# Performance work log

Hardware: AMD Instinct MI355X
Metric: run time of the kernel (lower is better)

The kernel has to match this reference:

```python
import jax, jax.numpy as jnp
import numpy as np

DIM = 1024
N_HEADS = 16


def setup_inputs() -> dict:
    key = jax.random.key(0)
    ks = jax.random.split(key, 7)
    x = jax.random.normal(ks[0], (2, 2048, DIM), dtype=jnp.float32)
    wq = jax.random.normal(ks[1], (DIM, DIM), dtype=jnp.float32) * 0.01
    wk = jax.random.normal(ks[2], (DIM, DIM), dtype=jnp.float32) * 0.01
    wv = jax.random.normal(ks[3], (DIM, DIM), dtype=jnp.float32) * 0.01
    wo = jax.random.normal(ks[4], (DIM, DIM), dtype=jnp.float32) * 0.01
    w1 = jax.random.normal(ks[5], (DIM, 4 * DIM), dtype=jnp.float32) * 0.01
    w2 = jax.random.normal(ks[6], (4 * DIM, DIM), dtype=jnp.float32) * 0.01
    return {"x": x, "wq": wq, "wk": wk, "wv": wv, "wo": wo, "w1": w1, "w2": w2}


def reference(x, wq, wk, wv, wo, w1, w2):
    bsz, seqlen, dim = x.shape
    head_dim = dim // N_HEADS
    # project and split heads: [b, h, s, d]
    q = (x @ wq).reshape(bsz, seqlen, N_HEADS, head_dim).transpose(0, 2, 1, 3)
    k = (x @ wk).reshape(bsz, seqlen, N_HEADS, head_dim).transpose(0, 2, 1, 3)
    v = (x @ wv).reshape(bsz, seqlen, N_HEADS, head_dim).transpose(0, 2, 1, 3)
    scale = head_dim ** (-0.5)
    # full [b, h, s, s] score matrix, as in the original module
    attn = jnp.einsum('bhqd,bhkd->bhqk', q, k) * scale
    attn = jax.nn.softmax(attn, axis=-1)
    out = jnp.einsum('bhqk,bhkd->bhqd', attn, v)
    out = out.transpose(0, 2, 1, 3).reshape(bsz, seqlen, dim)
    x = x + out @ wo
    h = jax.nn.relu(x @ w1)
    x = x + h @ w2
    return x
```

## Files before the change

### kernel.cpp

```cpp
#include <hip/hip_runtime.h>
#include <hip/hip_bf16.h>
#include <stdint.h>

typedef __attribute__((ext_vector_type(8))) short short8_t;
typedef __attribute__((ext_vector_type(4))) short short4_t;
typedef __attribute__((ext_vector_type(4))) float floatx4;

#define MTOT 4096
#define DIMV 1024
#define SEQ  2048
#define NH   16
#define HD   64
#define QKV_LD 3072
#define KVB 64
#define NKT (SEQ / KVB)

__device__ __forceinline__ floatx4 mfma16(short8_t a, short8_t b, floatx4 c) {
    return __builtin_amdgcn_mfma_f32_16x16x32_bf16(a, b, c, 0, 0, 0);
}

__device__ __forceinline__ void gload_lds16(const void* g, void* l) {
    __builtin_amdgcn_global_load_lds(
        (const __attribute__((address_space(1))) void*)g,
        (__attribute__((address_space(3))) void*)l,
        16, 0, 0);
}

__device__ __forceinline__ short bf16bits(float f) {
    return __builtin_bit_cast(short, __float2bfloat16(f));
}

__device__ __forceinline__ short8_t frag64(const __hip_bfloat16* base, int row, int col0) {
    int off = row * 64 + (((col0 >> 3) ^ (row & 7)) << 3);
    return *(const short8_t*)(base + off);
}


struct bf4 { __hip_bfloat16 a, b, c, d; };

__global__ void castbf(const float* __restrict__ x, __hip_bfloat16* __restrict__ o, int n4) {
    int i = blockIdx.x * 256 + threadIdx.x;
    if (i < n4) {
        const float4* xv = reinterpret_cast<const float4*>(x) + i;
        float4 v = *xv;
        bf4 r;
        r.a = __float2bfloat16(v.x); r.b = __float2bfloat16(v.y);
        r.c = __float2bfloat16(v.z); r.d = __float2bfloat16(v.w);
        *reinterpret_cast<bf4*>(o + (size_t)i * 4) = r;
    }
}

__global__ void wtrans(const float* __restrict__ w, __hip_bfloat16* __restrict__ wt,
                       int K, int N, float scale) {
    __shared__ float tile[32][33];
    int k0 = blockIdx.x * 32, n0 = blockIdx.y * 32;
    int tx = threadIdx.x & 31, ty = threadIdx.x >> 5;
    #pragma unroll
    for (int r = 0; r < 32; r += 8)
        tile[ty + r][tx] = w[(size_t)(k0 + ty + r) * N + n0 + tx];
    __syncthreads();
    #pragma unroll
    for (int r = 0; r < 32; r += 8)
        wt[(size_t)(n0 + ty + r) * K + k0 + tx] = __float2bfloat16(tile[tx][ty + r] * scale);
}

__global__ void vtrans(const __hip_bfloat16* __restrict__ v, int ld,
                       __hip_bfloat16* __restrict__ vt) {
    __shared__ __hip_bfloat16 tile[32][33];
    int s0 = blockIdx.x * 32;
    int c0 = blockIdx.y * 32;
    int tx = threadIdx.x & 31, ty = threadIdx.x >> 5;
    #pragma unroll
    for (int r = 0; r < 32; r += 8)
        tile[ty + r][tx] = v[(size_t)(s0 + ty + r) * ld + c0 + tx];
    __syncthreads();
    int b = s0 >> 11;
    int h = c0 >> 6;
    int d0 = c0 & 63;
    #pragma unroll
    for (int r = 0; r < 32; r += 8)
        vt[(size_t)((b * NH + h) * HD + d0 + ty + r) * SEQ + (s0 & 2047) + tx] = tile[tx][ty + r];
}

__global__ void combine2(const float* __restrict__ p0, const float* __restrict__ p1,
                         const float* __restrict__ resid, float* __restrict__ out, int n4) {
    int i = blockIdx.x * 256 + threadIdx.x;
    if (i < n4) {
        float4 a = reinterpret_cast<const float4*>(p0)[i];
        float4 b = reinterpret_cast<const float4*>(p1)[i];
        float4 c = reinterpret_cast<const float4*>(resid)[i];
        float4 r;
        r.x = a.x + b.x + c.x; r.y = a.y + b.y + c.y;
        r.z = a.z + b.z + c.z; r.w = a.w + b.w + c.w;
        reinterpret_cast<float4*>(out)[i] = r;
    }
}

template <int EPI>
__launch_bounds__(256)
__global__ void gemm_bt(const __hip_bfloat16* __restrict__ A,
                        const __hip_bfloat16* __restrict__ Bt,
                        int M, int N, int K, int lda, int ldb, float scale,
                        const float* __restrict__ resid,
                        float* __restrict__ outf,
                        __hip_bfloat16* __restrict__ outb, size_t zout) {
    __shared__ __align__(16) __hip_bfloat16 As[128 * 32];
    __shared__ __align__(16) __hip_bfloat16 Bs[128 * 32];
    A += (size_t)blockIdx.z * K;
    Bt += (size_t)blockIdx.z * K;
    outf += (size_t)blockIdx.z * zout;
    const int t = threadIdx.x;
    const int l = t & 63;
    const int w = t >> 6;
    const int wr = w >> 1, wc = w & 1;
    const int lrow = l & 15;
    const int lk = (l >> 4) << 3;
    const int li4 = (l >> 4) << 2;
    const int arow0 = blockIdx.x * 128;
    const int brow0 = blockIdx.y * 128;

    floatx4 acc[4][4];
    #pragma unroll
    for (int m = 0; m < 4; m++)
        #pragma unroll
        for (int n = 0; n < 4; n++)
            acc[m][n] = (floatx4){0.f, 0.f, 0.f, 0.f};

    const int nkt = K >> 5;
    const int sr = t >> 2, sc8 = (t & 3) << 3;
    for (int kt = 0; kt < nkt; ++kt) {
        __syncthreads();
        {
            const __hip_bfloat16* ga = A + (size_t)(arow0 + sr) * lda + kt * 32 + sc8;
            gload_lds16(ga,                    (char*)As + t * 16);
            gload_lds16(ga + (size_t)64 * lda, (char*)As + 4096 + t * 16);
            const __hip_bfloat16* gb = Bt + (size_t)(brow0 + sr) * ldb + kt * 32 + sc8;
            gload_lds16(gb,                    (char*)Bs + t * 16);
            gload_lds16(gb + (size_t)64 * ldb, (char*)Bs + 4096 + t * 16);
        }
        __syncthreads();
        short8_t af[4], bfr[4];
        #pragma unroll
        for (int m = 0; m < 4; m++)
            af[m] = *(const short8_t*)((const char*)As + (((wr << 6) + (m << 4) + lrow) << 6) + (lk << 1));
        #pragma unroll
        for (int n = 0; n < 4; n++)
            bfr[n] = *(const short8_t*)((const char*)Bs + (((wc << 6) + (n << 4) + lrow) << 6) + (lk << 1));
        #pragma unroll
        for (int m = 0; m < 4; m++)
            #pragma unroll
            for (int n = 0; n < 4; n++)
                acc[m][n] = mfma16(af[m], bfr[n], acc[m][n]);
    }

    #pragma unroll
    for (int m = 0; m < 4; m++) {
        #pragma unroll
        for (int n = 0; n < 4; n++) {
            int row = arow0 + (wr << 6) + (m << 4) + li4;
            int col = brow0 + (wc << 6) + (n << 4) + lrow;
            #pragma unroll
            for (int i = 0; i < 4; i++) {
                float vv = acc[m][n][i] * scale;
                size_t off = (size_t)(row + i) * N + col;
                if (EPI == 0) {
                    outb[off] = __float2bfloat16(vv);
                } else if (EPI == 1) {
                    outb[off] = __float2bfloat16(vv > 0.f ? vv : 0.f);
                } else if (EPI == 2) {
                    float f = vv + resid[off];
                    outf[off] = f;
                    outb[off] = __float2bfloat16(f);
                } else if (EPI == 3) {
                    outf[off] = vv + resid[off];
                } else {
                    outf[off] = vv;
                }
            }
        }
    }
}

__launch_bounds__(256, 3)
__global__ void attn_kernel(const __hip_bfloat16* __restrict__ qkv,
                            const __hip_bfloat16* __restrict__ vt,
                            __hip_bfloat16* __restrict__ o) {
    __shared__ __align__(16) __hip_bfloat16 Ks[2][KVB * 64];
    __shared__ __align__(16) __hip_bfloat16 Vs[2][KVB * 64];
    __shared__ __align__(16) __hip_bfloat16 Ps[128 * 64];
    const int t = threadIdx.x, l = t & 63, w = t >> 6;
    const int bh = blockIdx.y;
    const int b = bh >> 4, h = bh & 15;
    const int q0 = blockIdx.x * 128;
    const int lq = l & 15;
    const int lg = l >> 4;

    const __hip_bfloat16* qbase = qkv + (size_t)(b * SEQ + q0) * QKV_LD + h * HD;
    const __hip_bfloat16* kbase = qkv + (size_t)(b * SEQ) * QKV_LD + 1024 + h * HD;
    const __hip_bfloat16* vbase = vt + (size_t)(bh * HD) * SEQ;

    #pragma unroll
    for (int s = 0; s < 4; ++s) {
        int u = t + 256 * s;
        int r = u >> 3, c = (u & 7) ^ (r & 7);
        gload_lds16(qbase + (size_t)r * QKV_LD + c * 8, (char*)Ps + u * 16);
    }
    #pragma unroll
    for (int s = 0; s < 2; ++s) {
        int u = t + 256 * s;
        int r = u >> 3, c = (u & 7) ^ (r & 7);
        gload_lds16(kbase + (size_t)r * QKV_LD + c * 8, (char*)Ks[0] + u * 16);
        gload_lds16(vbase + (size_t)r * SEQ + c * 8,    (char*)Vs[0] + u * 16);
    }
    asm volatile("s_waitcnt vmcnt(0)" ::: "memory");
    __builtin_amdgcn_s_barrier();
    __builtin_amdgcn_sched_barrier(0);

    short8_t qf[2][2];
    #pragma unroll
    for (int m = 0; m < 2; m++)
        #pragma unroll
        for (int kc = 0; kc < 2; kc++)
            qf[m][kc] = frag64(Ps, (w << 5) + (m << 4) + lq, kc * 32 + lg * 8);
    asm volatile("s_waitcnt lgkmcnt(0)" ::: "memory");
    __builtin_amdgcn_s_barrier();
    __builtin_amdgcn_sched_barrier(0);

    float l_part[2] = {0.f, 0.f};
    floatx4 o_acc[2][4];
    #pragma unroll
    for (int m = 0; m < 2; m++)
        #pragma unroll
        for (int n = 0; n < 4; n++)
            o_acc[m][n] = (floatx4){0.f, 0.f, 0.f, 0.f};

    int cur = 0;
    for (int kt = 0; kt < NKT; ++kt) {
        if (kt + 1 < NKT) {
            int kv = (kt + 1) * KVB;
            #pragma unroll
            for (int s = 0; s < 2; ++s) {
                int u = t + 256 * s;
                int r = u >> 3, c = (u & 7) ^ (r & 7);
                gload_lds16(kbase + (size_t)(kv + r) * QKV_LD + c * 8,
                            (char*)Ks[cur ^ 1] + u * 16);
                gload_lds16(vbase + (size_t)r * SEQ + kv + c * 8,
                            (char*)Vs[cur ^ 1] + u * 16);
            }
        }

        const __hip_bfloat16* kc_base = Ks[cur];
        floatx4 sa[2][4];
        #pragma unroll
        for (int m = 0; m < 2; m++)
            #pragma unroll
            for (int n = 0; n < 4; n++)
                sa[m][n] = (floatx4){0.f, 0.f, 0.f, 0.f};
        #pragma unroll
        for (int n = 0; n < 4; n++) {
            #pragma unroll
            for (int kc = 0; kc < 2; kc++) {
                short8_t kf = frag64(kc_base, n * 16 + lq, kc * 32 + lg * 8);
                sa[0][n] = mfma16(kf, qf[0][kc], sa[0][n]);
                sa[1][n] = mfma16(kf, qf[1][kc], sa[1][n]);
            }
        }

        short4_t pk[2][4];
        #pragma unroll
        for (int m = 0; m < 2; m++) {
            #pragma unroll
            for (int n = 0; n < 4; n++) {
                float p0 = __expf(sa[m][n][0]);
                float p1 = __expf(sa[m][n][1]);
                float p2 = __expf(sa[m][n][2]);
                float p3 = __expf(sa[m][n][3]);
                l_part[m] += (p0 + p1) + (p2 + p3);
                short4_t pv;
                pv[0] = bf16bits(p0);
                pv[1] = bf16bits(p1);
                pv[2] = bf16bits(p2);
                pv[3] = bf16bits(p3);
                pk[m][n] = pv;
            }
        }

        #pragma unroll
        for (int m = 0; m < 2; m++) {
            int row = (w << 5) + (m << 4) + lq;
            #pragma unroll
            for (int n = 0; n < 4; n++) {
                int k0 = n * 16 + lg * 4;
                char* dst = (char*)Ps + row * 128 +
                            ((((k0 >> 3) ^ (row & 7)) << 4) | ((k0 & 4) << 1));
                *(short4_t*)dst = pk[m][n];
            }
        }
        asm volatile("s_waitcnt lgkmcnt(0)" ::: "memory");
        __builtin_amdgcn_s_barrier();
        __builtin_amdgcn_sched_barrier(0);

        const __hip_bfloat16* vc_base = Vs[cur];
        #pragma unroll
        for (int kc = 0; kc < 2; kc++) {
            short8_t pf0 = frag64(Ps, (w << 5) + lq,      kc * 32 + lg * 8);
            short8_t pf1 = frag64(Ps, (w << 5) + 16 + lq, kc * 32 + lg * 8);
            #pragma unroll
            for (int n = 0; n < 4; n++) {
                short8_t vf = frag64(vc_base, n * 16 + lq, kc * 32 + lg * 8);
                o_acc[0][n] = mfma16(pf0, vf, o_acc[0][n]);
                o_acc[1][n] = mfma16(pf1, vf, o_acc[1][n]);
            }
        }
        asm volatile("s_waitcnt vmcnt(0)" ::: "memory");
        __builtin_amdgcn_s_barrier();
        __builtin_amdgcn_sched_barrier(0);
        cur ^= 1;
    }

    __hip_bfloat16* obase = o + (size_t)(b * SEQ + q0) * DIMV + h * HD;
    #pragma unroll
    for (int m = 0; m < 2; m++) {
        float lr = l_part[m];
        lr += __shfl_xor(lr, 16, 64);
        lr += __shfl_xor(lr, 32, 64);
        #pragma unroll
        for (int i = 0; i < 4; i++) {
            float li = 1.0f / __shfl(lr, (lg << 2) + i, 16);
            int row = (w << 5) + (m << 4) + (lg << 2) + i;
            #pragma unroll
            for (int n = 0; n < 4; n++) {
                obase[(size_t)row * DIMV + n * 16 + lq] =
                    __float2bfloat16(o_acc[m][n][i] * li);
            }
        }
    }
}

extern "C" void kernel_launch(void* const* d_in, const int* in_sizes, int n_in,
                              void* d_out, int out_size, void* d_ws, size_t ws_size,
                              hipStream_t stream) {
    const float* x  = (const float*)d_in[0];
    const float* wq = (const float*)d_in[1];
    const float* wk = (const float*)d_in[2];
    const float* wv = (const float*)d_in[3];
    const float* wo = (const float*)d_in[4];
    const float* w1 = (const float*)d_in[5];
    const float* w2 = (const float*)d_in[6];
    float* outf = (float*)d_out;

    char* ws = (char*)d_ws;
    const size_t MB = (size_t)1 << 20;
    __hip_bfloat16* xb    = (__hip_bfloat16*)(ws + 0 * MB);
    __hip_bfloat16* wqkvt = (__hip_bfloat16*)(ws + 8 * MB);
    __hip_bfloat16* wot   = (__hip_bfloat16*)(ws + 14 * MB);
    __hip_bfloat16* w1t   = (__hip_bfloat16*)(ws + 16 * MB);
    __hip_bfloat16* w2t   = (__hip_bfloat16*)(ws + 24 * MB);
    __hip_bfloat16* qkvb  = (__hip_bfloat16*)(ws + 32 * MB);
    __hip_bfloat16* vtp   = (__hip_bfloat16*)(ws + 56 * MB);
    __hip_bfloat16* atb   = (__hip_bfloat16*)(ws + 64 * MB);
    __hip_bfloat16* x1b   = (__hip_bfloat16*)(ws + 72 * MB);
    __hip_bfloat16* hb    = (__hip_bfloat16*)(ws + 80 * MB);
    float* part0 = (float*)(ws + 32 * MB);

    castbf<<<dim3(4096), dim3(256), 0, stream>>>(x, xb, MTOT * DIMV / 4);
    wtrans<<<dim3(32, 32), dim3(256), 0, stream>>>(wq, wqkvt,               1024, 1024, 0.125f);
    wtrans<<<dim3(32, 32), dim3(256), 0, stream>>>(wk, wqkvt + 1024 * 1024, 1024, 1024, 1.0f);
    wtrans<<<dim3(32, 32), dim3(256), 0, stream>>>(wv, wqkvt + 2048 * 1024, 1024, 1024, 1.0f);
    wtrans<<<dim3(32, 32), dim3(256), 0, stream>>>(wo, wot, 1024, 1024, 1.0f);
    wtrans<<<dim3(32, 128), dim3(256), 0, stream>>>(w1, w1t, 1024, 4096, 1.0f);
    wtrans<<<dim3(128, 32), dim3(256), 0, stream>>>(w2, w2t, 4096, 1024, 1.0f);

    gemm_bt<0><<<dim3(32, 24), dim3(256), 0, stream>>>(xb, wqkvt, MTOT, QKV_LD, 1024,
                                                       1024, 1024, 1.0f, nullptr, nullptr, qkvb, 0);
    vtrans<<<dim3(128, 32), dim3(256), 0, stream>>>(qkvb + 2048, QKV_LD, vtp);

    attn_kernel<<<dim3(16, 32), dim3(256), 0, stream>>>(qkvb, vtp, atb);

    gemm_bt<2><<<dim3(32, 8), dim3(256), 0, stream>>>(atb, wot, MTOT, 1024, 1024,
                                                      1024, 1024, 1.0f, x, outf, x1b, 0);
    gemm_bt<1><<<dim3(32, 32), dim3(256), 0, stream>>>(x1b, w1t, MTOT, 4096, 1024,
                                                       1024, 1024, 1.0f, nullptr, nullptr, hb, 0);
    gemm_bt<4><<<dim3(32, 8, 2), dim3(256), 0, stream>>>(hb, w2t, MTOT, 1024, 2048,
                                                         4096, 4096, 1.0f, nullptr, part0, nullptr,
                                                         (size_t)MTOT * 1024);
    combine2<<<dim3(4096), dim3(256), 0, stream>>>(part0, part0 + (size_t)MTOT * 1024,
                                                   outf, outf, MTOT * 1024 / 4);
}
```

Measured before the change: 362.0 us.

## Double-buffer GEMM LDS tiles and merge prep kernels into one launch

The GEMM main loop now uses two LDS buffers, so the next K-tile's global-to-LDS load is issued before computing on the current tile, leaving one barrier per iteration instead of two. The seven prep kernels (x cast and six weight transposes) are merged into a single launch that dispatches on block index. The aim is to hide global load latency behind MFMA work and to cut launch overhead. LDS use per block doubles, which may reduce occupancy.

```diff
diff --git a/kernel.cpp b/kernel.cpp
--- a/kernel.cpp
+++ b/kernel.cpp
@@ -35,26 +35,37 @@
     return *(const short8_t*)(base + off);
 }
 
-
 struct bf4 { __hip_bfloat16 a, b, c, d; };
 
-__global__ void castbf(const float* __restrict__ x, __hip_bfloat16* __restrict__ o, int n4) {
-    int i = blockIdx.x * 256 + threadIdx.x;
-    if (i < n4) {
+__global__ void prep_all(const float* __restrict__ x,
+                         const float* __restrict__ wq, const float* __restrict__ wk,
+                         const float* __restrict__ wv, const float* __restrict__ wo,
+                         const float* __restrict__ w1, const float* __restrict__ w2,
+                         __hip_bfloat16* __restrict__ xb,
+                         __hip_bfloat16* __restrict__ wqkvt, __hip_bfloat16* __restrict__ wot,
+                         __hip_bfloat16* __restrict__ w1t, __hip_bfloat16* __restrict__ w2t) {
+    __shared__ float tile[32][33];
+    int bid = blockIdx.x;
+    int t = threadIdx.x;
+    if (bid >= 12288) {
+        int i = (bid - 12288) * 256 + t;
         const float4* xv = reinterpret_cast<const float4*>(x) + i;
         float4 v = *xv;
         bf4 r;
         r.a = __float2bfloat16(v.x); r.b = __float2bfloat16(v.y);
         r.c = __float2bfloat16(v.z); r.d = __float2bfloat16(v.w);
-        *reinterpret_cast<bf4*>(o + (size_t)i * 4) = r;
-    }
-}
-
-__global__ void wtrans(const float* __restrict__ w, __hip_bfloat16* __restrict__ wt,
-                       int K, int N, float scale) {
-    __shared__ float tile[32][33];
-    int k0 = blockIdx.x * 32, n0 = blockIdx.y * 32;
-    int tx = threadIdx.x & 31, ty = threadIdx.x >> 5;
+        *reinterpret_cast<bf4*>(xb + (size_t)i * 4) = r;
+        return;
+    }
+    const float* w; __hip_bfloat16* wt; int K, N, K32, tau; float scale = 1.0f;
+    if (bid < 1024)      { w = wq; wt = wqkvt;                 K = 1024; N = 1024; K32 = 32;  tau = bid;        scale = 0.125f; }
+    else if (bid < 2048) { w = wk; wt = wqkvt + 1024 * 1024;   K = 1024; N = 1024; K32 = 32;  tau = bid - 1024; }
+    else if (bid < 3072) { w = wv; wt = wqkvt + 2048 * 1024;   K = 1024; N = 1024; K32 = 32;  tau = bid - 2048; }
+    else if (bid < 4096) { w = wo; wt = wot;                   K = 1024; N = 1024; K32 = 32;  tau = bid - 3072; }
+    else if (bid < 8192) { w = w1; wt = w1t;                   K = 1024; N = 4096; K32 = 32;  tau = bid - 4096; }
+    else                 { w = w2; wt = w2t;                   K = 4096; N = 1024; K32 = 128; tau = bid - 8192; }
+    int k0 = (tau % K32) * 32, n0 = (tau / K32) * 32;
+    int tx = t & 31, ty = t >> 5;
     #pragma unroll
     for (int r = 0; r < 32; r += 8)
         tile[ty + r][tx] = w[(size_t)(k0 + ty + r) * N + n0 + tx];
@@ -104,8 +115,8 @@
                         const float* __restrict__ resid,
                         float* __restrict__ outf,
                         __hip_bfloat16* __restrict__ outb, size_t zout) {
-    __shared__ __align__(16) __hip_bfloat16 As[128 * 32];
-    __shared__ __align__(16) __hip_bfloat16 Bs[128 * 32];
+    __shared__ __align__(16) __hip_bfloat16 As[2][128 * 32];
+    __shared__ __align__(16) __hip_bfloat16 Bs[2][128 * 32];
     A += (size_t)blockIdx.z * K;
     Bt += (size_t)blockIdx.z * K;
     outf += (size_t)blockIdx.z * zout;
@@ -128,29 +139,43 @@
 
     const int nkt = K >> 5;
     const int sr = t >> 2, sc8 = (t & 3) << 3;
+    const __hip_bfloat16* ga0 = A + (size_t)(arow0 + sr) * lda + sc8;
+    const __hip_bfloat16* gb0 = Bt + (size_t)(brow0 + sr) * ldb + sc8;
+
+    gload_lds16(ga0,                    (char*)As[0] + t * 16);
+    gload_lds16(ga0 + (size_t)64 * lda, (char*)As[0] + 4096 + t * 16);
+    gload_lds16(gb0,                    (char*)Bs[0] + t * 16);
+    gload_lds16(gb0 + (size_t)64 * ldb, (char*)Bs[0] + 4096 + t * 16);
+    asm volatile("s_waitcnt vmcnt(0)" ::: "memory");
+    __builtin_amdgcn_s_barrier();
+    __builtin_amdgcn_sched_barrier(0);
+
+    int cur = 0;
     for (int kt = 0; kt < nkt; ++kt) {
-        __syncthreads();
-        {
-            const __hip_bfloat16* ga = A + (size_t)(arow0 + sr) * lda + kt * 32 + sc8;
-            gload_lds16(ga,                    (char*)As + t * 16);
-            gload_lds16(ga + (size_t)64 * lda, (char*)As + 4096 + t * 16);
-            const __hip_bfloat16* gb = Bt + (size_t)(brow0 + sr) * ldb + kt * 32 + sc8;
-            gload_lds16(gb,                    (char*)Bs + t * 16);
-            gload_lds16(gb + (size_t)64 * ldb, (char*)Bs + 4096 + t * 16);
-        }
-        __syncthreads();
+        if (kt + 1 < nkt) {
+            const __hip_bfloat16* ga = ga0 + (kt + 1) * 32;
+            const __hip_bfloat16* gb = gb0 + (kt + 1) * 32;
+            gload_lds16(ga,                    (char*)As[cur ^ 1] + t * 16);
+            gload_lds16(ga + (size_t)64 * lda, (char*)As[cur ^ 1] + 4096 + t * 16);
+            gload_lds16(gb,                    (char*)Bs[cur ^ 1] + t * 16);
+            gload_lds16(gb + (size_t)64 * ldb, (char*)Bs[cur ^ 1] + 4096 + t * 16);
+        }
         short8_t af[4], bfr[4];
         #pragma unroll
         for (int m = 0; m < 4; m++)
-            af[m] = *(const short8_t*)((const char*)As + (((wr << 6) + (m << 4) + lrow) << 6) + (lk << 1));
+            af[m] = *(const short8_t*)((const char*)As[cur] + (((wr << 6) + (m << 4) + lrow) << 6) + (lk << 1));
         #pragma unroll
         for (int n = 0; n < 4; n++)
-            bfr[n] = *(const short8_t*)((const char*)Bs + (((wc << 6) + (n << 4) + lrow) << 6) + (lk << 1));
+            bfr[n] = *(const short8_t*)((const char*)Bs[cur] + (((wc << 6) + (n << 4) + lrow) << 6) + (lk << 1));
         #pragma unroll
         for (int m = 0; m < 4; m++)
             #pragma unroll
             for (int n = 0; n < 4; n++)
                 acc[m][n] = mfma16(af[m], bfr[n], acc[m][n]);
+        asm volatile("s_waitcnt vmcnt(0)" ::: "memory");
+        __builtin_amdgcn_s_barrier();
+        __builtin_amdgcn_sched_barrier(0);
+        cur ^= 1;
     }
 
     #pragma unroll
@@ -363,13 +388,8 @@
     __hip_bfloat16* hb    = (__hip_bfloat16*)(ws + 80 * MB);
     float* part0 = (float*)(ws + 32 * MB);
 
-    castbf<<<dim3(4096), dim3(256), 0, stream>>>(x, xb, MTOT * DIMV / 4);
-    wtrans<<<dim3(32, 32), dim3(256), 0, stream>>>(wq, wqkvt,               1024, 1024, 0.125f);
-    wtrans<<<dim3(32, 32), dim3(256), 0, stream>>>(wk, wqkvt + 1024 * 1024, 1024, 1024, 1.0f);
-    wtrans<<<dim3(32, 32), dim3(256), 0, stream>>>(wv, wqkvt + 2048 * 1024, 1024, 1024, 1.0f);
-    wtrans<<<dim3(32, 32), dim3(256), 0, stream>>>(wo, wot, 1024, 1024, 1.0f);
-    wtrans<<<dim3(32, 128), dim3(256), 0, stream>>>(w1, w1t, 1024, 4096, 1.0f);
-    wtrans<<<dim3(128, 32), dim3(256), 0, stream>>>(w2, w2t, 4096, 1024, 1.0f);
+    prep_all<<<dim3(16384), dim3(256), 0, stream>>>(x, wq, wk, wv, wo, w1, w2,
+                                                    xb, wqkvt, wot, w1t, w2t);
 
     gemm_bt<0><<<dim3(32, 24), dim3(256), 0, stream>>>(xb, wqkvt, MTOT, QKV_LD, 1024,
                                                        1024, 1024, 1.0f, nullptr, nullptr, qkvb, 0);
```

Measured after the change: 333.3 us. 7.9% less time.
